# Performance work log

Hardware: AMD Instinct MI355X
Metric: run time of the kernel (lower is better)

Reference implementation:

```python
import jax, jax.numpy as jnp
import numpy as np
from math import factorial, sqrt

LMAX = 2
SH = (LMAX + 1) ** 2  # 9 real spherical-harmonic components
N_ATOMS = 1000
N_EDGES = 10000
N_BASIS = 128
N_RADIAL = 20


def _cg_complex(l1, m1, l2, m2, l3, m3):
    # Racah formula for complex Clebsch-Gordan <l1 m1 l2 m2 | l3 m3>
    if m3 != m1 + m2 or not (abs(l1 - l2) <= l3 <= l1 + l2):
        return 0.0
    pre = sqrt((2 * l3 + 1) * factorial(l3 + l1 - l2) * factorial(l3 - l1 + l2)
               * factorial(l1 + l2 - l3) / factorial(l1 + l2 + l3 + 1))
    pre *= sqrt(factorial(l3 + m3) * factorial(l3 - m3) * factorial(l1 - m1)
                * factorial(l1 + m1) * factorial(l2 - m2) * factorial(l2 + m2))
    kmin = max(0, l2 - l3 - m1, l1 - l3 + m2)
    kmax = min(l1 + l2 - l3, l1 - m1, l2 + m2)
    s = 0.0
    for k in range(kmin, kmax + 1):
        s += (-1) ** k / (factorial(k) * factorial(l1 + l2 - l3 - k)
                          * factorial(l1 - m1 - k) * factorial(l2 + m2 - k)
                          * factorial(l3 - l2 + m1 + k) * factorial(l3 - l1 - m2 + k))
    return pre * s


def _u_c2r(l):
    # complex -> real spherical-harmonic change of basis, rows real m, cols complex m
    U = np.zeros((2 * l + 1, 2 * l + 1), dtype=np.complex128)
    U[l, l] = 1.0
    for m in range(1, l + 1):
        U[l + m, l + m] = (-1) ** m / np.sqrt(2.0)
        U[l + m, l - m] = 1.0 / np.sqrt(2.0)
        U[l - m, l - m] = 1j / np.sqrt(2.0)
        U[l - m, l + m] = -1j * (-1) ** m / np.sqrt(2.0)
    return U


def _generate_cg_rsh(lmax):
    # real-SH Clebsch-Gordan tensor with parity invariance (odd l1+l2+l3 zeroed)
    S = (lmax + 1) ** 2
    cg = np.zeros((S, S, S))
    for l1 in range(lmax + 1):
        for l2 in range(lmax + 1):
            for l3 in range(lmax + 1):
                if (l1 + l2 + l3) % 2 == 1 or not (abs(l1 - l2) <= l3 <= l1 + l2):
                    continue
                block = np.zeros((2 * l1 + 1, 2 * l2 + 1, 2 * l3 + 1), dtype=np.complex128)
                for m1 in range(-l1, l1 + 1):
                    for m2 in range(-l2, l2 + 1):
                        m3 = m1 + m2
                        if abs(m3) <= l3:
                            block[m1 + l1, m2 + l2, m3 + l3] = _cg_complex(l1, m1, l2, m2, l3, m3)
                rb = np.einsum('abc,ia,jb,kc->ijk', block, _u_c2r(l1), _u_c2r(l2), np.conj(_u_c2r(l3)))
                cg[l1 * l1:(l1 + 1) ** 2, l2 * l2:(l2 + 1) ** 2, l3 * l3:(l3 + 1) ** 2] = np.real(rb)
    cg[np.abs(cg) < 1e-12] = 0.0
    return cg


_CG_T = _generate_cg_rsh(LMAX)
_I1, _I2, _IO = np.nonzero(_CG_T)
CG = jnp.asarray(_CG_T[_I1, _I2, _IO].astype(np.float32))  # [P] nonzero CG values
IDX_IN_1 = jnp.asarray(_I1)
IDX_IN_2 = jnp.asarray(_I2)
IDX_OUT = jnp.asarray(_IO)
_LIDX = np.repeat(np.arange(LMAX + 1), 2 * np.arange(LMAX + 1) + 1)  # degree l per SH index
WIDX = jnp.asarray(_LIDX[_I1])  # filter degree per CG path (schnetpack Widx)


def setup_inputs() -> dict:
    key = jax.random.key(0)
    ks = jax.random.split(key, 7)
    return {
        "x": jax.random.normal(ks[0], (N_ATOMS, SH, N_BASIS), jnp.float32),
        "radial_ij": jax.random.normal(ks[1], (N_EDGES, N_RADIAL), jnp.float32),
        "dir_ij": jax.random.normal(ks[2], (N_EDGES, SH), jnp.float32),
        "cutoff_ij": jax.random.uniform(ks[3], (N_EDGES, 1), jnp.float32),
        "Wf": jax.random.normal(ks[4], (N_RADIAL, (LMAX + 1) * N_BASIS), jnp.float32) * 0.1,
        "bf": jnp.zeros(((LMAX + 1) * N_BASIS,), jnp.float32),
        "idx_i": jax.random.randint(ks[5], (N_EDGES,), 0, N_ATOMS),
        "idx_j": jax.random.randint(ks[6], (N_EDGES,), 0, N_ATOMS),
        "n_atoms": N_ATOMS,
    }


def reference(x, radial_ij, dir_ij, cutoff_ij, Wf, bf, idx_i, idx_j, n_atoms):
    E = radial_ij.shape[0]
    # radial filter: Dense(n_radial -> (lmax+1)*C) * cutoff, gathered per CG path by degree l
    Wij = (radial_ij @ Wf + bf) * cutoff_ij                     # [E,(L+1)*C]
    Wij = Wij.reshape(E, LMAX + 1, N_BASIS)[:, WIDX]            # [E,P,C]
    xj = x[idx_j][:, IDX_IN_2]                                  # gather neighbor feats: [E,P,C]
    v = Wij * dir_ij[:, IDX_IN_1, None] * CG[None, :, None] * xj  # [E,P,C]
    # scatter_add over CG paths -> output SH index
    yij = jnp.zeros((E, SH, N_BASIS), v.dtype).at[:, IDX_OUT, :].add(v)  # [E,S,C]
    # scatter_add over edges -> receiving atom
    y = jax.ops.segment_sum(yij, idx_i, num_segments=n_atoms)   # [n_atoms,S,C]
    return y
```

## Files before the change

kernel.cpp:

```cpp
#include <hip/hip_runtime.h>


#define SH_N 9
#define NB 128
#define NR 20
#define NSUB 4
#define NT2 (NSUB * NB)
#define CAPL 128
#define EB 8

namespace cgc {

struct CD { double re, im; };
constexpr CD cmul(CD x, CD y) { return {x.re * y.re - x.im * y.im, x.re * y.im + x.im * y.re}; }
constexpr CD cadd(CD x, CD y) { return {x.re + y.re, x.im + y.im}; }
constexpr CD cconj(CD x) { return {x.re, -x.im}; }

constexpr double FACT[10] = {1., 1., 2., 6., 24., 120., 720., 5040., 40320., 362880.};

constexpr double csqrt(double a) {
    if (a <= 0.0) return 0.0;
    double x = a < 1.0 ? 1.0 : a;
    for (int i = 0; i < 40; ++i) x = 0.5 * (x + a / x);
    return x;
}

constexpr double cg_complex(int l1, int m1, int l2, int m2, int l3, int m3) {
    if (m3 != m1 + m2) return 0.0;
    int dl = l1 > l2 ? l1 - l2 : l2 - l1;
    if (l3 < dl || l3 > l1 + l2) return 0.0;
    double pre = csqrt((2.0 * l3 + 1.0) * FACT[l3 + l1 - l2] * FACT[l3 - l1 + l2]
                       * FACT[l1 + l2 - l3] / FACT[l1 + l2 + l3 + 1]);
    pre = pre * csqrt(FACT[l3 + m3] * FACT[l3 - m3] * FACT[l1 - m1] * FACT[l1 + m1]
                      * FACT[l2 - m2] * FACT[l2 + m2]);
    int kmin = 0;
    if (l2 - l3 - m1 > kmin) kmin = l2 - l3 - m1;
    if (l1 - l3 + m2 > kmin) kmin = l1 - l3 + m2;
    int kmax = l1 + l2 - l3;
    if (l1 - m1 < kmax) kmax = l1 - m1;
    if (l2 + m2 < kmax) kmax = l2 + m2;
    double s = 0.0;
    for (int k = kmin; k <= kmax; ++k) {
        double term = 1.0 / (FACT[k] * FACT[l1 + l2 - l3 - k] * FACT[l1 - m1 - k]
                             * FACT[l2 + m2 - k] * FACT[l3 - l2 + m1 + k] * FACT[l3 - l1 - m2 + k]);
        s += (k & 1) ? -term : term;
    }
    return pre * s;
}

struct U5 { CD m[5][5]; };
constexpr U5 u_c2r(int l) {
    U5 u{};
    const double isq = csqrt(0.5);
    u.m[l][l] = {1.0, 0.0};
    for (int mm = 1; mm <= l; ++mm) {
        double sgn = (mm & 1) ? -1.0 : 1.0;
        u.m[l + mm][l + mm] = {sgn * isq, 0.0};
        u.m[l + mm][l - mm] = {isq, 0.0};
        u.m[l - mm][l - mm] = {0.0, isq};
        u.m[l - mm][l + mm] = {0.0, -sgn * isq};
    }
    return u;
}

struct CGTab { float v[SH_N][SH_N][SH_N]; };

constexpr CGTab build_cg() {
    CGTab t{};
    for (int l1 = 0; l1 <= 2; ++l1)
    for (int l2 = 0; l2 <= 2; ++l2)
    for (int l3 = 0; l3 <= 2; ++l3) {
        int dl = l1 > l2 ? l1 - l2 : l2 - l1;
        if (((l1 + l2 + l3) & 1) || l3 < dl || l3 > l1 + l2) continue;
        U5 U1 = u_c2r(l1), U2 = u_c2r(l2), U3 = u_c2r(l3);
        const int n1 = 2 * l1 + 1, n2 = 2 * l2 + 1, n3 = 2 * l3 + 1;
        double blk[5][5][5] = {};
        for (int a = 0; a < n1; ++a)
        for (int b = 0; b < n2; ++b) {
            int m1 = a - l1, m2 = b - l2, m3 = m1 + m2;
            if (m3 < -l3 || m3 > l3) continue;
            blk[a][b][m3 + l3] = cg_complex(l1, m1, l2, m2, l3, m3);
        }
        for (int i = 0; i < n1; ++i)
        for (int j = 0; j < n2; ++j)
        for (int k = 0; k < n3; ++k) {
            CD s{0.0, 0.0};
            for (int a = 0; a < n1; ++a) {
                if (U1.m[i][a].re == 0.0 && U1.m[i][a].im == 0.0) continue;
                for (int b = 0; b < n2; ++b) {
                    if (U2.m[j][b].re == 0.0 && U2.m[j][b].im == 0.0) continue;
                    int m3 = (a - l1) + (b - l2);
                    if (m3 < -l3 || m3 > l3) continue;
                    double B = blk[a][b][m3 + l3];
                    if (B == 0.0) continue;
                    CD u3 = cconj(U3.m[k][m3 + l3]);
                    if (u3.re == 0.0 && u3.im == 0.0) continue;
                    CD term = cmul(cmul(U1.m[i][a], U2.m[j][b]), u3);
                    s = cadd(s, CD{term.re * B, term.im * B});
                }
            }
            double v = s.re;
            if (v < 1e-12 && v > -1e-12) v = 0.0;
            t.v[l1 * l1 + i][l2 * l2 + j][l3 * l3 + k] = (float)v;
        }
    }
    return t;
}

}

static constexpr cgc::CGTab CGT = cgc::build_cg();

__device__ __forceinline__ float sel_w(int a, float w0, float w1, float w2) {
    return (a == 0) ? w0 : ((a < 4) ? w1 : w2);
}


__global__ void __launch_bounds__(NB)
radial_kernel(const float* __restrict__ radial,
              const float* __restrict__ cutoff,
              const float* __restrict__ Wf,
              const float* __restrict__ bf,
              float* __restrict__ W,
              int E) {
    const int c = threadIdx.x;
    float wreg[NR * 3];
#pragma unroll
    for (int r = 0; r < NR; ++r)
#pragma unroll
        for (int l = 0; l < 3; ++l)
            wreg[r * 3 + l] = Wf[r * 3 * NB + l * NB + c];
    const float b0 = bf[c], b1 = bf[NB + c], b2 = bf[2 * NB + c];

    const int e0 = blockIdx.x * EB;
#pragma unroll
    for (int i = 0; i < EB; ++i) {
        const int e = e0 + i;
        if (e >= E) return;
        const float* rad = radial + (size_t)e * NR;
        float a0 = b0, a1 = b1, a2 = b2;
#pragma unroll
        for (int r = 0; r < NR; ++r) {
            const float rv = rad[r];
            a0 = fmaf(rv, wreg[r * 3 + 0], a0);
            a1 = fmaf(rv, wreg[r * 3 + 1], a1);
            a2 = fmaf(rv, wreg[r * 3 + 2], a2);
        }
        const float cut = cutoff[e];
        float* wp = W + (size_t)e * (3 * NB) + c;
        wp[0]       = a0 * cut;
        wp[NB]      = a1 * cut;
        wp[2 * NB]  = a2 * cut;
    }
}


struct Ld { float xr[SH_N]; float w0, w1, w2; };

__device__ __forceinline__ void load_edge(Ld& L, float (&d)[SH_N], int e,
        const float* __restrict__ x, const float* __restrict__ W,
        const float* __restrict__ dir, const int* __restrict__ idx_j, int c) {
    const int aj = idx_j[e];
    const float* xp = x + (size_t)aj * (SH_N * NB) + c;
#pragma unroll
    for (int k = 0; k < SH_N; ++k) L.xr[k] = xp[k * NB];
    const float* wp = W + (size_t)e * (3 * NB) + c;
    L.w0 = wp[0]; L.w1 = wp[NB]; L.w2 = wp[2 * NB];
    const float* dp = dir + (size_t)e * SH_N;
#pragma unroll
    for (int k = 0; k < SH_N; ++k) d[k] = dp[k];
}

__device__ __forceinline__ void comp_edge(const Ld& L, const float (&d)[SH_N],
                                          float (&acc)[SH_N]) {
#pragma unroll
    for (int ai = 0; ai < SH_N; ++ai) {
        const float daw = d[ai] * sel_w(ai, L.w0, L.w1, L.w2);
#pragma unroll
        for (int bi = 0; bi < SH_N; ++bi) {
            const float g = daw * L.xr[bi];
#pragma unroll
            for (int o = 0; o < SH_N; ++o)
                if (CGT.v[ai][bi][o] != 0.0f)
                    acc[o] = fmaf(CGT.v[ai][bi][o], g, acc[o]);
        }
    }
}

__global__ void __launch_bounds__(NT2)
so3_atom_kernel(const float* __restrict__ x,
                const float* __restrict__ W,
                const float* __restrict__ dir,
                const int* __restrict__ idx_i,
                const int* __restrict__ idx_j,
                float* __restrict__ y,
                int E) {
    const int a    = blockIdx.x;
    const int tid  = threadIdx.x;
    const int sub  = tid >> 7;
    const int c    = tid & (NB - 1);
    const int lane = tid & 63;
    const int wid  = tid >> 6;

    __shared__ int s_list[CAPL];
    __shared__ int s_wsum[NT2 / 64];
    __shared__ int s_m;

    unsigned long long mask = 0ull;
    int cnt = 0;
    const int E4 = E >> 2;
    const bool fast_scan = (4 * ((E4 + NT2 - 1) / NT2) <= 60);
    if (fast_scan) {
        const int4* p4 = (const int4*)idx_i;
        int b = 0;
        for (int k4 = tid; k4 < E4; k4 += NT2, ++b) {
            const int4 q = p4[k4];
            unsigned long long h = (unsigned long long)(q.x == a)
                                 | ((unsigned long long)(q.y == a) << 1)
                                 | ((unsigned long long)(q.z == a) << 2)
                                 | ((unsigned long long)(q.w == a) << 3);
            mask |= h << (4 * b);
        }
        const int kt = 4 * E4 + tid;
        if (tid < (E & 3) && kt < E && idx_i[kt] == a)
            mask |= 1ull << (60 + tid);
        cnt = __popcll(mask);
    } else {
        for (int k = tid; k < E; k += NT2) cnt += (idx_i[k] == a);
    }

    int v = cnt;
#pragma unroll
    for (int d = 1; d < 64; d <<= 1) {
        int u = __shfl_up(v, d);
        if (lane >= d) v += u;
    }
    if (lane == 63) s_wsum[wid] = v;
    __syncthreads();
    if (tid == 0) {
        int t = 0;
#pragma unroll
        for (int w = 0; w < NT2 / 64; ++w) { int q = s_wsum[w]; s_wsum[w] = t; t += q; }
        s_m = t;
    }
    __syncthreads();
    int off = s_wsum[wid] + v - cnt;

    if (fast_scan) {
        unsigned long long mm = mask;
        while (mm) {
            const int p = __ffsll(mm) - 1;
            mm &= mm - 1;
            int k;
            if (p >= 60) k = 4 * E4 + (p - 60);
            else         k = 4 * (tid + (p >> 2) * NT2) + (p & 3);
            if (off < CAPL) s_list[off] = k;
            ++off;
        }
    } else if (cnt > 0) {
        for (int k = tid; k < E; k += NT2)
            if (idx_i[k] == a) { if (off < CAPL) s_list[off] = k; ++off; }
    }
    __syncthreads();
    const int m = (s_m < CAPL) ? s_m : CAPL;

    float acc[SH_N];
#pragma unroll
    for (int o = 0; o < SH_N; ++o) acc[o] = 0.f;

    int ie = sub;
    if (ie < m) {
        Ld LA, LB;
        float dA[SH_N], dB[SH_N];
        {
            const int eA = __builtin_amdgcn_readfirstlane(s_list[ie]);
            load_edge(LA, dA, eA, x, W, dir, idx_j, c);
        }
        for (;;) {
            int ien = ie + NSUB;
            if (ien < m) {
                const int eB = __builtin_amdgcn_readfirstlane(s_list[ien]);
                load_edge(LB, dB, eB, x, W, dir, idx_j, c);
                comp_edge(LA, dA, acc);
                ie = ien; ien += NSUB;
                if (ien < m) {
                    const int eA = __builtin_amdgcn_readfirstlane(s_list[ien]);
                    load_edge(LA, dA, eA, x, W, dir, idx_j, c);
                    comp_edge(LB, dB, acc);
                    ie = ien;
                } else {
                    comp_edge(LB, dB, acc);
                    break;
                }
            } else {
                comp_edge(LA, dA, acc);
                break;
            }
        }
    }

    __shared__ float s_red[NSUB][SH_N * NB];
#pragma unroll
    for (int o = 0; o < SH_N; ++o) s_red[sub][o * NB + c] = acc[o];
    __syncthreads();
    float* yo = y + (size_t)a * (SH_N * NB);
    for (int oc = tid; oc < SH_N * NB; oc += NT2)
        yo[oc] = s_red[0][oc] + s_red[1][oc] + s_red[2][oc] + s_red[3][oc];
}


__global__ void __launch_bounds__(NT2)
so3_atom_kernel_lds(const float* __restrict__ x,
                    const float* __restrict__ radial,
                    const float* __restrict__ dir,
                    const float* __restrict__ cutoff,
                    const float* __restrict__ Wf,
                    const float* __restrict__ bf,
                    const int* __restrict__ idx_i,
                    const int* __restrict__ idx_j,
                    float* __restrict__ y,
                    int E) {
    const int a    = blockIdx.x;
    const int tid  = threadIdx.x;
    const int sub  = tid >> 7;
    const int c    = tid & (NB - 1);
    const int lane = tid & 63;
    const int wid  = tid >> 6;

    __shared__ int s_list[CAPL];
    __shared__ int s_wsum[NT2 / 64];
    __shared__ int s_m;
    __shared__ float s_wf[NR * 3 * NB];

    for (int idx = tid; idx < NR * 3 * NB; idx += NT2) s_wf[idx] = Wf[idx];

    unsigned long long mask = 0ull;
    int cnt = 0;
    const int E4 = E >> 2;
    const bool fast_scan = (4 * ((E4 + NT2 - 1) / NT2) <= 60);
    if (fast_scan) {
        const int4* p4 = (const int4*)idx_i;
        int b = 0;
        for (int k4 = tid; k4 < E4; k4 += NT2, ++b) {
            const int4 q = p4[k4];
            unsigned long long h = (unsigned long long)(q.x == a)
                                 | ((unsigned long long)(q.y == a) << 1)
                                 | ((unsigned long long)(q.z == a) << 2)
                                 | ((unsigned long long)(q.w == a) << 3);
            mask |= h << (4 * b);
        }
        const int kt = 4 * E4 + tid;
        if (tid < (E & 3) && kt < E && idx_i[kt] == a)
            mask |= 1ull << (60 + tid);
        cnt = __popcll(mask);
    } else {
        for (int k = tid; k < E; k += NT2) cnt += (idx_i[k] == a);
    }

    int v = cnt;
#pragma unroll
    for (int d = 1; d < 64; d <<= 1) {
        int u = __shfl_up(v, d);
        if (lane >= d) v += u;
    }
    if (lane == 63) s_wsum[wid] = v;
    __syncthreads();
    if (tid == 0) {
        int t = 0;
#pragma unroll
        for (int w = 0; w < NT2 / 64; ++w) { int q = s_wsum[w]; s_wsum[w] = t; t += q; }
        s_m = t;
    }
    __syncthreads();
    int off = s_wsum[wid] + v - cnt;
    if (fast_scan) {
        unsigned long long mm = mask;
        while (mm) {
            const int p = __ffsll(mm) - 1;
            mm &= mm - 1;
            int k;
            if (p >= 60) k = 4 * E4 + (p - 60);
            else         k = 4 * (tid + (p >> 2) * NT2) + (p & 3);
            if (off < CAPL) s_list[off] = k;
            ++off;
        }
    } else if (cnt > 0) {
        for (int k = tid; k < E; k += NT2)
            if (idx_i[k] == a) { if (off < CAPL) s_list[off] = k; ++off; }
    }
    __syncthreads();
    const int m = (s_m < CAPL) ? s_m : CAPL;

    float acc[SH_N];
#pragma unroll
    for (int o = 0; o < SH_N; ++o) acc[o] = 0.f;
    const float b0 = bf[c], b1 = bf[NB + c], b2 = bf[2 * NB + c];

    for (int ie = sub; ie < m; ie += NSUB) {
        const int e = __builtin_amdgcn_readfirstlane(s_list[ie]);
        const int aj = idx_j[e];
        float xr[SH_N];
        const float* xp = x + (size_t)aj * (SH_N * NB) + c;
#pragma unroll
        for (int k = 0; k < SH_N; ++k) xr[k] = xp[k * NB];
        const float* rad = radial + (size_t)e * NR;
        float a0 = b0, a1 = b1, a2 = b2;
#pragma unroll
        for (int r = 0; r < NR; ++r) {
            const float rv = rad[r];
            a0 = fmaf(rv, s_wf[(r * 3 + 0) * NB + c], a0);
            a1 = fmaf(rv, s_wf[(r * 3 + 1) * NB + c], a1);
            a2 = fmaf(rv, s_wf[(r * 3 + 2) * NB + c], a2);
        }
        const float cut = cutoff[e];
        const float w0 = a0 * cut, w1 = a1 * cut, w2 = a2 * cut;
        const float* dp = dir + (size_t)e * SH_N;
#pragma unroll
        for (int ai = 0; ai < SH_N; ++ai) {
            const float daw = dp[ai] * sel_w(ai, w0, w1, w2);
#pragma unroll
            for (int bi = 0; bi < SH_N; ++bi) {
                const float g = daw * xr[bi];
#pragma unroll
                for (int o = 0; o < SH_N; ++o)
                    if (CGT.v[ai][bi][o] != 0.0f)
                        acc[o] = fmaf(CGT.v[ai][bi][o], g, acc[o]);
            }
        }
    }

    __shared__ float s_red[NSUB][SH_N * NB];
#pragma unroll
    for (int o = 0; o < SH_N; ++o) s_red[sub][o * NB + c] = acc[o];
    __syncthreads();
    float* yo = y + (size_t)a * (SH_N * NB);
    for (int oc = tid; oc < SH_N * NB; oc += NT2)
        yo[oc] = s_red[0][oc] + s_red[1][oc] + s_red[2][oc] + s_red[3][oc];
}


extern "C" void kernel_launch(void* const* d_in, const int* in_sizes, int n_in,
                              void* d_out, int out_size, void* d_ws, size_t ws_size,
                              hipStream_t stream) {
    const float* x      = (const float*)d_in[0];
    const float* radial = (const float*)d_in[1];
    const float* dir    = (const float*)d_in[2];
    const float* cutoff = (const float*)d_in[3];
    const float* Wf     = (const float*)d_in[4];
    const float* bf     = (const float*)d_in[5];
    const int*   idx_i  = (const int*)d_in[6];
    const int*   idx_j  = (const int*)d_in[7];
    float* y = (float*)d_out;
    const int E = in_sizes[6];
    const int n_atoms = out_size / (SH_N * NB);

    const size_t needW = (size_t)E * 3 * NB * sizeof(float);
    if (ws_size >= needW) {
        float* W = (float*)d_ws;
        radial_kernel<<<(E + EB - 1) / EB, NB, 0, stream>>>(radial, cutoff, Wf, bf, W, E);
        so3_atom_kernel<<<n_atoms, NT2, 0, stream>>>(x, W, dir, idx_i, idx_j, y, E);
    } else {
        so3_atom_kernel_lds<<<n_atoms, NT2, 0, stream>>>(x, radial, dir, cutoff,
                                                         Wf, bf, idx_i, idx_j, y, E);
    }
}
```

Before: 31.04 us.

## Halve edge sub-groups per block and deepen per-thread load prefetch to two edges

Each block now uses two edge sub-groups of 128 threads instead of four, so each thread handles more edges. The ping-pong load/compute loop becomes a three-stage rotating prefetch that keeps two edges' gathers in flight, and a launch-bounds occupancy hint of 4 is added. The aim is better memory latency hiding and a cheaper final reduction, at the cost of more registers and less per-block parallelism for atoms with many edges. The hidden edge-list scan code may still assume 512 threads per block (constants such as p>=60 and NT2/64), which could affect correctness.

New measurement: 33.50 us. 7.9% more time.

```diff
diff --git a/kernel.cpp b/kernel.cpp
--- a/kernel.cpp
+++ b/kernel.cpp
@@ -4,7 +4,7 @@
 #define SH_N 9
 #define NB 128
 #define NR 20
-#define NSUB 4
+#define NSUB 2
 #define NT2 (NSUB * NB)
 #define CAPL 128
 #define EB 8
@@ -155,30 +155,29 @@
 }
 
 
-struct Ld { float xr[SH_N]; float w0, w1, w2; };
-
-__device__ __forceinline__ void load_edge(Ld& L, float (&d)[SH_N], int e,
+struct St { float xr[SH_N]; float d[SH_N]; float w0, w1, w2; };
+
+__device__ __forceinline__ void load_st(St& s, int e,
         const float* __restrict__ x, const float* __restrict__ W,
         const float* __restrict__ dir, const int* __restrict__ idx_j, int c) {
     const int aj = idx_j[e];
     const float* xp = x + (size_t)aj * (SH_N * NB) + c;
 #pragma unroll
-    for (int k = 0; k < SH_N; ++k) L.xr[k] = xp[k * NB];
+    for (int k = 0; k < SH_N; ++k) s.xr[k] = xp[k * NB];
+    const float* dp = dir + (size_t)e * SH_N;
+#pragma unroll
+    for (int k = 0; k < SH_N; ++k) s.d[k] = dp[k];
     const float* wp = W + (size_t)e * (3 * NB) + c;
-    L.w0 = wp[0]; L.w1 = wp[NB]; L.w2 = wp[2 * NB];
-    const float* dp = dir + (size_t)e * SH_N;
-#pragma unroll
-    for (int k = 0; k < SH_N; ++k) d[k] = dp[k];
-}
-
-__device__ __forceinline__ void comp_edge(const Ld& L, const float (&d)[SH_N],
-                                          float (&acc)[SH_N]) {
+    s.w0 = wp[0]; s.w1 = wp[NB]; s.w2 = wp[2 * NB];
+}
+
+__device__ __forceinline__ void comp_st(const St& s, float (&acc)[SH_N]) {
 #pragma unroll
     for (int ai = 0; ai < SH_N; ++ai) {
-        const float daw = d[ai] * sel_w(ai, L.w0, L.w1, L.w2);
+        const float daw = s.d[ai] * sel_w(ai, s.w0, s.w1, s.w2);
 #pragma unroll
         for (int bi = 0; bi < SH_N; ++bi) {
-            const float g = daw * L.xr[bi];
+            const float g = daw * s.xr[bi];
 #pragma unroll
             for (int o = 0; o < SH_N; ++o)
                 if (CGT.v[ai][bi][o] != 0.0f)
@@ -187,7 +186,7 @@
     }
 }
 
-__global__ void __launch_bounds__(NT2)
+__global__ void __launch_bounds__(NT2, 4)
 so3_atom_kernel(const float* __restrict__ x,
                 const float* __restrict__ W,
                 const float* __restrict__ dir,
@@ -268,35 +267,19 @@
 #pragma unroll
     for (int o = 0; o < SH_N; ++o) acc[o] = 0.f;
 
-    int ie = sub;
-    if (ie < m) {
-        Ld LA, LB;
-        float dA[SH_N], dB[SH_N];
-        {
-            const int eA = __builtin_amdgcn_readfirstlane(s_list[ie]);
-            load_edge(LA, dA, eA, x, W, dir, idx_j, c);
-        }
-        for (;;) {
-            int ien = ie + NSUB;
-            if (ien < m) {
-                const int eB = __builtin_amdgcn_readfirstlane(s_list[ien]);
-                load_edge(LB, dB, eB, x, W, dir, idx_j, c);
-                comp_edge(LA, dA, acc);
-                ie = ien; ien += NSUB;
-                if (ien < m) {
-                    const int eA = __builtin_amdgcn_readfirstlane(s_list[ien]);
-                    load_edge(LA, dA, eA, x, W, dir, idx_j, c);
-                    comp_edge(LB, dB, acc);
-                    ie = ien;
-                } else {
-                    comp_edge(LB, dB, acc);
-                    break;
-                }
-            } else {
-                comp_edge(LA, dA, acc);
-                break;
-            }
-        }
+    {
+        St A, B, C;
+        const int iA = sub, iB = sub + NSUB;
+        const bool hA = iA < m, hB = iB < m;
+        if (hA) load_st(A, __builtin_amdgcn_readfirstlane(s_list[iA]), x, W, dir, idx_j, c);
+        if (hB) load_st(B, __builtin_amdgcn_readfirstlane(s_list[iB]), x, W, dir, idx_j, c);
+        for (int i = sub + 2 * NSUB; i < m; i += NSUB) {
+            load_st(C, __builtin_amdgcn_readfirstlane(s_list[i]), x, W, dir, idx_j, c);
+            comp_st(A, acc);
+            A = B; B = C;
+        }
+        if (hA) comp_st(A, acc);
+        if (hB) comp_st(B, acc);
     }
 
     __shared__ float s_red[NSUB][SH_N * NB];
@@ -305,7 +288,7 @@
     __syncthreads();
     float* yo = y + (size_t)a * (SH_N * NB);
     for (int oc = tid; oc < SH_N * NB; oc += NT2)
-        yo[oc] = s_red[0][oc] + s_red[1][oc] + s_red[2][oc] + s_red[3][oc];
+        yo[oc] = s_red[0][oc] + s_red[1][oc];
 }
 
 
@@ -435,7 +418,7 @@
     __syncthreads();
     float* yo = y + (size_t)a * (SH_N * NB);
     for (int oc = tid; oc < SH_N * NB; oc += NT2)
-        yo[oc] = s_red[0][oc] + s_red[1][oc] + s_red[2][oc] + s_red[3][oc];
+        yo[oc] = s_red[0][oc] + s_red[1][oc];
 }
 
 
```
